# Kernel tuning notes

Measured on AMD Instinct MI355X. Metric: run time of the kernel, lower is better.

The kernel has to match this reference:

```python
import jax, jax.numpy as jnp
import numpy as np

N_TREES, N_LEAVES, PATH_LEN, N_NODES, D, B = 10, 16, 5, 31, 256, 4096


def _local_paths():
    # root-to-leaf paths of a full binary tree, depth 4: 31 nodes, 16 leaves, path len 5
    return np.array([[0, 1 + l // 8, 3 + l // 4, 7 + l // 2, 15 + l]
                     for l in range(N_LEAVES)], np.int32)


def setup_inputs() -> dict:
    key = jax.random.key(0)
    k1, k2, k3, k4, k5, k6 = jax.random.split(key, 6)
    # one activated leaf per tree -> multi-hot cross_features (B, N_TREES*N_LEAVES)
    leaf = jax.random.randint(k1, (B, N_TREES), 0, N_LEAVES)
    cross = jnp.zeros((B, N_TREES, N_LEAVES), jnp.float32)
    cross = cross.at[jnp.arange(B)[:, None], jnp.arange(N_TREES)[None, :], leaf].set(1.0)
    cross_features = cross.reshape(B, N_TREES * N_LEAVES)
    # learned params: node embedding table + single-layer LSTM (torch init scale 1/sqrt(D))
    emb = jax.random.normal(k2, (N_TREES * N_NODES, D), jnp.float32) * 0.02
    s = 1.0 / np.sqrt(D)
    W_ih = jax.random.uniform(k3, (4 * D, D), jnp.float32, -s, s)
    W_hh = jax.random.uniform(k4, (4 * D, D), jnp.float32, -s, s)
    b_ih = jax.random.uniform(k5, (4 * D,), jnp.float32, -s, s)
    b_hh = jax.random.uniform(k6, (4 * D,), jnp.float32, -s, s)
    return {"cross_features": cross_features, "emb": emb, "W_ih": W_ih,
            "W_hh": W_hh, "b_ih": b_ih, "b_hh": b_hh}


def reference(cross_features, emb, W_ih, W_hh, b_ih, b_hh):
    # global path node ids per (tree, leaf): [T, L, P]
    gpaths = jnp.asarray(_local_paths())[None, :, :] + \
        (jnp.arange(N_TREES, dtype=jnp.int32) * N_NODES)[:, None, None]
    # activated leaf per tree (exactly one hot per 16-leaf block)
    leaf = jnp.argmax(cross_features.reshape(B, N_TREES, N_LEAVES), axis=-1)  # [B, T]
    node_ids = gpaths[jnp.arange(N_TREES)[None, :], leaf]                     # [B, T, P]
    x = emb[node_ids].reshape(B * N_TREES, PATH_LEN, D)                       # packed paths
    # precompute input projections for all steps: [N, P, 4D]
    xg = jnp.einsum('npd,gd->npg', x, W_ih) + (b_ih + b_hh)

    def step(carry, xt):
        h, c = carry
        g = xt + h @ W_hh.T
        i, f, gg, o = jnp.split(g, 4, axis=-1)  # torch gate order: i, f, g, o
        c = jax.nn.sigmoid(f) * c + jax.nn.sigmoid(i) * jnp.tanh(gg)
        h = jax.nn.sigmoid(o) * jnp.tanh(c)
        return (h, c), None

    n = B * N_TREES
    h0 = jnp.zeros((n, D), x.dtype)
    (h, _), _ = jax.lax.scan(step, (h0, h0), jnp.swapaxes(xg, 0, 1))
    return h.reshape(B, N_TREES, D)
```

## Files before the change

### kernel.cpp

```cpp
#include <hip/hip_runtime.h>

#define NT 10
#define NL 16
#define NN 31
#define DD 256
#define NB 4096

__device__ unsigned g_gen[NT * 16];

__device__ __forceinline__ float sigf(float x)   { return 1.0f / (1.0f + __expf(-x)); }
__device__ __forceinline__ float tanh_f(float x) { return 2.0f / (1.0f + __expf(-2.0f*x)) - 1.0f; }

__device__ __forceinline__ void pub64(unsigned long long* p, unsigned tag, float v) {
    union { float f; unsigned u; } c; c.f = v;
    __hip_atomic_store(p, ((unsigned long long)tag << 32) | c.u,
                       __ATOMIC_RELAXED, __HIP_MEMORY_SCOPE_AGENT);
}
__device__ __forceinline__ unsigned long long ld64(const unsigned long long* p) {
    return __hip_atomic_load(p, __ATOMIC_RELAXED, __HIP_MEMORY_SCOPE_AGENT);
}

__global__ __launch_bounds__(256) void k_treelstm(
    const float* __restrict__ emb, const float* __restrict__ Wih,
    const float* __restrict__ Whh, const float* __restrict__ bih,
    const float* __restrict__ bhh,
    unsigned long long* __restrict__ hx0, unsigned long long* __restrict__ hx1,
    unsigned long long* __restrict__ hx2, unsigned long long* __restrict__ hx3,
    float* __restrict__ h4g)
{
    __shared__ float es [NN * DD];
    __shared__ float ps [8 * DD];
    __shared__ float xsl[NN * 64];
    __shared__ float hs [8 * DD];
    __shared__ float cbuf[2 * 128];
    __shared__ float bsl[64];
    __shared__ unsigned stag;

    const int tid  = threadIdx.x;
    const int t    = blockIdx.x >> 4;
    const int dt   = blockIdx.x & 15;
    const int kq   = tid >> 6;
    const int w    = tid & 63;
    const int gate = w >> 4;
    const int col  = w & 15;
    const int grow = gate * DD + dt * 16 + col;

    if (tid == 0) {
        unsigned G = __hip_atomic_load(&g_gen[t * 16 + dt],
            __ATOMIC_RELAXED, __HIP_MEMORY_SCOPE_AGENT);
        __hip_atomic_store(&g_gen[t * 16 + dt], G + 1u,
            __ATOMIC_RELAXED, __HIP_MEMORY_SCOPE_AGENT);
        stag = G + 1u;
    }
    if (tid < 64) {
        int g2 = tid >> 4, c3 = tid & 15;
        int r2 = g2 * DD + dt * 16 + c3;
        bsl[tid] = bih[r2] + bhh[r2];
    }

    const float4* Wi4 = (const float4*)Wih + (size_t)grow * 64 + kq * 16;
    const float4* Wh4 = (const float4*)Whh + (size_t)grow * 64 + kq * 16;
    float4 wih[16], whh[16];
    #pragma unroll
    for (int j = 0; j < 16; ++j) { wih[j] = Wi4[j]; whh[j] = Wh4[j]; }

    const float4* emb4 = (const float4*)emb + (size_t)t * NN * 64;
    float4* es4 = (float4*)es;
    #pragma unroll
    for (int r = 0; r < 8; ++r) {
        int idx = tid + 256 * r;
        if (idx < NN * 64) es4[idx] = emb4[idx];
    }
    __syncthreads();
    const unsigned tag = stag;

    auto xbatch = [&](int n0, int nn) {
        __syncthreads();
        float acc[8];
        #pragma unroll
        for (int m = 0; m < 8; ++m) acc[m] = 0.f;
        #pragma unroll
        for (int j = 0; j < 16; ++j) {
            float4 wv = wih[j];
            #pragma unroll
            for (int m = 0; m < 8; ++m) {
                if (m < nn) {
                    float4 h = es4[(n0 + m) * 64 + kq * 16 + j];
                    acc[m] = fmaf(wv.x, h.x, fmaf(wv.y, h.y,
                             fmaf(wv.z, h.z, fmaf(wv.w, h.w, acc[m]))));
                }
            }
        }
        #pragma unroll
        for (int m = 0; m < 8; ++m)
            if (m < nn) ps[m * DD + kq * 64 + w] = acc[m];
        __syncthreads();
        #pragma unroll
        for (int rep = 0; rep < 2; ++rep) {
            int idx = tid + 256 * rep;
            if (idx < nn * 64) {
                int m = idx >> 6, w2 = idx & 63;
                xsl[(n0 + m) * 64 + w2] =
                      ps[m * DD +   0 + w2] + ps[m * DD +  64 + w2]
                    + ps[m * DD + 128 + w2] + ps[m * DD + 192 + w2] + bsl[w2];
            }
        }
        __syncthreads();
    };

    xbatch(0, 1);
    if (tid < 16) {
        float xi  = xsl[ 0 + tid];
        float xgg = xsl[32 + tid];
        float xo  = xsl[48 + tid];
        float c0 = sigf(xi) * tanh_f(xgg);
        float h0 = sigf(xo) * tanh_f(c0);
        cbuf[tid] = c0;
        pub64(hx0 + (size_t)t * DD + dt * 16 + tid, tag, h0);
    }

    xbatch(1, 6);

    {
        const unsigned long long* src = hx0 + (size_t)t * DD;
        unsigned long long v = ld64(src + tid);
        while ((unsigned)(v >> 32) != tag) {
            __builtin_amdgcn_s_sleep(1);
            v = ld64(src + tid);
        }
        union { unsigned u; float f; } cv; cv.u = (unsigned)v;
        hs[tid] = cv.f;
    }
    __syncthreads();

    const unsigned long long* hin[3] = { hx1, hx2, hx3 };
    unsigned long long* hout[3] = { hx1, hx2, hx3 };

    #pragma unroll
    for (int s = 1; s <= 4; ++s) {
        const int L = 1 << (s - 1);

        if (s > 1) {
            const unsigned long long* src = hin[s - 2] + (size_t)t * L * DD;
            unsigned long long v[8];
            #pragma unroll
            for (int r = 0; r < L; ++r) v[r] = ld64(src + tid + 256 * r);
            #pragma unroll
            for (int r = 0; r < L; ++r) {
                while ((unsigned)(v[r] >> 32) != tag) {
                    __builtin_amdgcn_s_sleep(1);
                    v[r] = ld64(src + tid + 256 * r);
                }
                union { unsigned u; float f; } cv; cv.u = (unsigned)v[r];
                hs[tid + 256 * r] = cv.f;
            }
            __syncthreads();
        }

        const float4* hs4 = (const float4*)hs;
        float acc[8];
        #pragma unroll
        for (int p = 0; p < 8; ++p) acc[p] = 0.f;
        #pragma unroll
        for (int j = 0; j < 16; ++j) {
            float4 wv = whh[j];
            #pragma unroll
            for (int p = 0; p < L; ++p) {
                float4 h = hs4[p * 64 + kq * 16 + j];
                acc[p] = fmaf(wv.x, h.x, fmaf(wv.y, h.y,
                         fmaf(wv.z, h.z, fmaf(wv.w, h.w, acc[p]))));
            }
        }
        #pragma unroll
        for (int p = 0; p < L; ++p) ps[p * DD + kq * 64 + w] = acc[p];
        __syncthreads();

        if (tid < 32 * L) {
            const int p  = tid >> 5;
            const int c2 = tid & 15;
            const int q  = tid >> 4;
            float g0 = 0.f, g1 = 0.f, g2 = 0.f, g3 = 0.f;
            #pragma unroll
            for (int k = 0; k < 4; ++k) {
                const float* pp = ps + p * DD + k * 64;
                g0 += pp[ 0 + c2]; g1 += pp[16 + c2];
                g2 += pp[32 + c2]; g3 += pp[48 + c2];
            }
            const int node = (1 << s) - 1 + q;
            const float* xp = xsl + node * 64;
            float gi = g0 + xp[ 0 + c2];
            float gf = g1 + xp[16 + c2];
            float gg = g2 + xp[32 + c2];
            float go = g3 + xp[48 + c2];
            float cin = cbuf[((s - 1) & 1) * 128 + p * 16 + c2];
            float cn  = sigf(gf) * cin + sigf(gi) * tanh_f(gg);
            float hn  = sigf(go) * tanh_f(cn);
            if (s < 4) {
                cbuf[(s & 1) * 128 + q * 16 + c2] = cn;
                pub64(hout[s - 1] + (size_t)(t * 2 * L + q) * DD
                                  + dt * 16 + c2, tag, hn);
            } else {
                h4g[(size_t)(t * NL + q) * DD + dt * 16 + c2] = hn;
            }
        }

        if (s == 1)      xbatch( 7, 8);
        else if (s == 2) xbatch(15, 8);
        else if (s == 3) xbatch(23, 8);
    }
}

__global__ __launch_bounds__(256) void k_scatter(
    const float* __restrict__ cross, const float* __restrict__ htab,
    float* __restrict__ out)
{
    const int tid  = threadIdx.x;
    const int wave = tid >> 6;
    const int lane = tid & 63;
    const int r = blockIdx.x * 4 + wave;
    const int b = r / NT;
    const int t = r - b * NT;

    float v = 0.f;
    if (lane < NL) v = cross[(size_t)b * (NT * NL) + t * NL + lane];
    unsigned long long m = __ballot(v > 0.5f);
    int leaf = m ? (int)__builtin_ctzll(m) : 0;
    int p = t * NL + leaf;

    const float4* h4 = (const float4*)htab;
    float4* o4 = (float4*)out;
    o4[(size_t)r * 64 + lane] = h4[(size_t)p * 64 + lane];
}

extern "C" void kernel_launch(void* const* d_in, const int* in_sizes, int n_in,
                              void* d_out, int out_size, void* d_ws, size_t ws_size,
                              hipStream_t stream)
{
    const float* cross = (const float*)d_in[0];
    const float* emb   = (const float*)d_in[1];
    const float* Wih   = (const float*)d_in[2];
    const float* Whh   = (const float*)d_in[3];
    const float* bih   = (const float*)d_in[4];
    const float* bhh   = (const float*)d_in[5];
    float* out = (float*)d_out;

    unsigned long long* hx0 = (unsigned long long*)d_ws;
    unsigned long long* hx1 = hx0 + (size_t)NT * DD;
    unsigned long long* hx2 = hx1 + (size_t)2 * NT * DD;
    unsigned long long* hx3 = hx2 + (size_t)4 * NT * DD;
    float* h4g = (float*)(hx3 + (size_t)8 * NT * DD);

    hipLaunchKernelGGL(k_treelstm, dim3(160), dim3(256), 0, stream,
                       emb, Wih, Whh, bih, bhh, hx0, hx1, hx2, hx3, h4g);
    hipLaunchKernelGGL(k_scatter, dim3(10240), dim3(256), 0, stream,
                       cross, h4g, out);
}
```

Baseline: 101.3 us.

## Fuse tree-LSTM and leaf scatter into one persistent kernel with tagged flags

Merges the recurrence kernel and the gather/scatter kernel into a single launch. The first 160 blocks run the tree LSTM and publish the final leaf hidden states with generation tags, and 320 extra blocks decode the active leaves and spin on those tags before writing the output. This removes the second launch and the gap between kernels, and lets the output writes overlap the recurrence tail. It depends on all 480 blocks being co-resident, since spinning blocks could otherwise starve the producers, and it doubles the bytes read for the gathered states because each value carries a 64-bit tag.

```diff
diff --git a/kernel.cpp b/kernel.cpp
--- a/kernel.cpp
+++ b/kernel.cpp
@@ -5,8 +5,10 @@
 #define NN 31
 #define DD 256
 #define NB 4096
+#define NSB 320
 
 __device__ unsigned g_gen[NT * 16];
+__device__ unsigned g_sgen[NSB];
 
 __device__ __forceinline__ float sigf(float x)   { return 1.0f / (1.0f + __expf(-x)); }
 __device__ __forceinline__ float tanh_f(float x) { return 2.0f / (1.0f + __expf(-2.0f*x)) - 1.0f; }
@@ -19,217 +21,256 @@
 __device__ __forceinline__ unsigned long long ld64(const unsigned long long* p) {
     return __hip_atomic_load(p, __ATOMIC_RELAXED, __HIP_MEMORY_SCOPE_AGENT);
 }
-
-__global__ __launch_bounds__(256) void k_treelstm(
-    const float* __restrict__ emb, const float* __restrict__ Wih,
-    const float* __restrict__ Whh, const float* __restrict__ bih,
-    const float* __restrict__ bhh,
+__device__ __forceinline__ float payload(unsigned long long w) {
+    union { unsigned u; float f; } c; c.u = (unsigned)w; return c.f;
+}
+
+__global__ __launch_bounds__(256, 2) void k_fused(
+    const float* __restrict__ cross, const float* __restrict__ emb,
+    const float* __restrict__ Wih,   const float* __restrict__ Whh,
+    const float* __restrict__ bih,   const float* __restrict__ bhh,
     unsigned long long* __restrict__ hx0, unsigned long long* __restrict__ hx1,
     unsigned long long* __restrict__ hx2, unsigned long long* __restrict__ hx3,
-    float* __restrict__ h4g)
-{
-    __shared__ float es [NN * DD];
-    __shared__ float ps [8 * DD];
-    __shared__ float xsl[NN * 64];
-    __shared__ float hs [8 * DD];
-    __shared__ float cbuf[2 * 128];
-    __shared__ float bsl[64];
-    __shared__ unsigned stag;
-
-    const int tid  = threadIdx.x;
-    const int t    = blockIdx.x >> 4;
-    const int dt   = blockIdx.x & 15;
-    const int kq   = tid >> 6;
-    const int w    = tid & 63;
-    const int gate = w >> 4;
-    const int col  = w & 15;
-    const int grow = gate * DD + dt * 16 + col;
-
-    if (tid == 0) {
-        unsigned G = __hip_atomic_load(&g_gen[t * 16 + dt],
-            __ATOMIC_RELAXED, __HIP_MEMORY_SCOPE_AGENT);
-        __hip_atomic_store(&g_gen[t * 16 + dt], G + 1u,
-            __ATOMIC_RELAXED, __HIP_MEMORY_SCOPE_AGENT);
-        stag = G + 1u;
-    }
-    if (tid < 64) {
-        int g2 = tid >> 4, c3 = tid & 15;
-        int r2 = g2 * DD + dt * 16 + c3;
-        bsl[tid] = bih[r2] + bhh[r2];
-    }
-
-    const float4* Wi4 = (const float4*)Wih + (size_t)grow * 64 + kq * 16;
-    const float4* Wh4 = (const float4*)Whh + (size_t)grow * 64 + kq * 16;
-    float4 wih[16], whh[16];
-    #pragma unroll
-    for (int j = 0; j < 16; ++j) { wih[j] = Wi4[j]; whh[j] = Wh4[j]; }
-
-    const float4* emb4 = (const float4*)emb + (size_t)t * NN * 64;
-    float4* es4 = (float4*)es;
-    #pragma unroll
-    for (int r = 0; r < 8; ++r) {
-        int idx = tid + 256 * r;
-        if (idx < NN * 64) es4[idx] = emb4[idx];
-    }
-    __syncthreads();
-    const unsigned tag = stag;
-
-    auto xbatch = [&](int n0, int nn) {
-        __syncthreads();
-        float acc[8];
-        #pragma unroll
-        for (int m = 0; m < 8; ++m) acc[m] = 0.f;
-        #pragma unroll
-        for (int j = 0; j < 16; ++j) {
-            float4 wv = wih[j];
-            #pragma unroll
-            for (int m = 0; m < 8; ++m) {
-                if (m < nn) {
-                    float4 h = es4[(n0 + m) * 64 + kq * 16 + j];
-                    acc[m] = fmaf(wv.x, h.x, fmaf(wv.y, h.y,
-                             fmaf(wv.z, h.z, fmaf(wv.w, h.w, acc[m]))));
-                }
-            }
-        }
-        #pragma unroll
-        for (int m = 0; m < 8; ++m)
-            if (m < nn) ps[m * DD + kq * 64 + w] = acc[m];
-        __syncthreads();
-        #pragma unroll
-        for (int rep = 0; rep < 2; ++rep) {
-            int idx = tid + 256 * rep;
-            if (idx < nn * 64) {
-                int m = idx >> 6, w2 = idx & 63;
-                xsl[(n0 + m) * 64 + w2] =
-                      ps[m * DD +   0 + w2] + ps[m * DD +  64 + w2]
-                    + ps[m * DD + 128 + w2] + ps[m * DD + 192 + w2] + bsl[w2];
-            }
-        }
-        __syncthreads();
-    };
-
-    xbatch(0, 1);
-    if (tid < 16) {
-        float xi  = xsl[ 0 + tid];
-        float xgg = xsl[32 + tid];
-        float xo  = xsl[48 + tid];
-        float c0 = sigf(xi) * tanh_f(xgg);
-        float h0 = sigf(xo) * tanh_f(c0);
-        cbuf[tid] = c0;
-        pub64(hx0 + (size_t)t * DD + dt * 16 + tid, tag, h0);
-    }
-
-    xbatch(1, 6);
-
-    {
-        const unsigned long long* src = hx0 + (size_t)t * DD;
-        unsigned long long v = ld64(src + tid);
-        while ((unsigned)(v >> 32) != tag) {
-            __builtin_amdgcn_s_sleep(1);
-            v = ld64(src + tid);
-        }
-        union { unsigned u; float f; } cv; cv.u = (unsigned)v;
-        hs[tid] = cv.f;
-    }
-    __syncthreads();
-
-    const unsigned long long* hin[3] = { hx1, hx2, hx3 };
-    unsigned long long* hout[3] = { hx1, hx2, hx3 };
-
-    #pragma unroll
-    for (int s = 1; s <= 4; ++s) {
-        const int L = 1 << (s - 1);
-
-        if (s > 1) {
-            const unsigned long long* src = hin[s - 2] + (size_t)t * L * DD;
-            unsigned long long v[8];
-            #pragma unroll
-            for (int r = 0; r < L; ++r) v[r] = ld64(src + tid + 256 * r);
-            #pragma unroll
-            for (int r = 0; r < L; ++r) {
-                while ((unsigned)(v[r] >> 32) != tag) {
-                    __builtin_amdgcn_s_sleep(1);
-                    v[r] = ld64(src + tid + 256 * r);
-                }
-                union { unsigned u; float f; } cv; cv.u = (unsigned)v[r];
-                hs[tid + 256 * r] = cv.f;
-            }
-            __syncthreads();
-        }
-
-        const float4* hs4 = (const float4*)hs;
-        float acc[8];
-        #pragma unroll
-        for (int p = 0; p < 8; ++p) acc[p] = 0.f;
-        #pragma unroll
-        for (int j = 0; j < 16; ++j) {
-            float4 wv = whh[j];
-            #pragma unroll
-            for (int p = 0; p < L; ++p) {
-                float4 h = hs4[p * 64 + kq * 16 + j];
-                acc[p] = fmaf(wv.x, h.x, fmaf(wv.y, h.y,
-                         fmaf(wv.z, h.z, fmaf(wv.w, h.w, acc[p]))));
-            }
-        }
-        #pragma unroll
-        for (int p = 0; p < L; ++p) ps[p * DD + kq * 64 + w] = acc[p];
-        __syncthreads();
-
-        if (tid < 32 * L) {
-            const int p  = tid >> 5;
-            const int c2 = tid & 15;
-            const int q  = tid >> 4;
-            float g0 = 0.f, g1 = 0.f, g2 = 0.f, g3 = 0.f;
-            #pragma unroll
-            for (int k = 0; k < 4; ++k) {
-                const float* pp = ps + p * DD + k * 64;
-                g0 += pp[ 0 + c2]; g1 += pp[16 + c2];
-                g2 += pp[32 + c2]; g3 += pp[48 + c2];
-            }
-            const int node = (1 << s) - 1 + q;
-            const float* xp = xsl + node * 64;
-            float gi = g0 + xp[ 0 + c2];
-            float gf = g1 + xp[16 + c2];
-            float gg = g2 + xp[32 + c2];
-            float go = g3 + xp[48 + c2];
-            float cin = cbuf[((s - 1) & 1) * 128 + p * 16 + c2];
-            float cn  = sigf(gf) * cin + sigf(gi) * tanh_f(gg);
-            float hn  = sigf(go) * tanh_f(cn);
-            if (s < 4) {
-                cbuf[(s & 1) * 128 + q * 16 + c2] = cn;
-                pub64(hout[s - 1] + (size_t)(t * 2 * L + q) * DD
-                                  + dt * 16 + c2, tag, hn);
-            } else {
-                h4g[(size_t)(t * NL + q) * DD + dt * 16 + c2] = hn;
-            }
-        }
-
-        if (s == 1)      xbatch( 7, 8);
-        else if (s == 2) xbatch(15, 8);
-        else if (s == 3) xbatch(23, 8);
-    }
-}
-
-__global__ __launch_bounds__(256) void k_scatter(
-    const float* __restrict__ cross, const float* __restrict__ htab,
+    unsigned long long* __restrict__ hx4,
     float* __restrict__ out)
 {
-    const int tid  = threadIdx.x;
-    const int wave = tid >> 6;
-    const int lane = tid & 63;
-    const int r = blockIdx.x * 4 + wave;
-    const int b = r / NT;
-    const int t = r - b * NT;
-
-    float v = 0.f;
-    if (lane < NL) v = cross[(size_t)b * (NT * NL) + t * NL + lane];
-    unsigned long long m = __ballot(v > 0.5f);
-    int leaf = m ? (int)__builtin_ctzll(m) : 0;
-    int p = t * NL + leaf;
-
-    const float4* h4 = (const float4*)htab;
-    float4* o4 = (float4*)out;
-    o4[(size_t)r * 64 + lane] = h4[(size_t)p * 64 + lane];
+    __shared__ float smem[14336];
+    __shared__ unsigned stag;
+    const int tid = threadIdx.x;
+    const int bid = blockIdx.x;
+
+    if (bid < 160) {
+        float* es   = smem;
+        float* ps   = smem + 7936;
+        float* xsl  = smem + 9984;
+        float* hs   = smem + 11968;
+        float* cbuf = smem + 14016;
+        float* bsl  = smem + 14272;
+        float4* es4 = (float4*)es;
+
+        const int t    = bid >> 4;
+        const int dt   = bid & 15;
+        const int kq   = tid >> 6;
+        const int w    = tid & 63;
+        const int gate = w >> 4;
+        const int col  = w & 15;
+        const int grow = gate * DD + dt * 16 + col;
+
+        if (tid == 0) {
+            unsigned G = __hip_atomic_load(&g_gen[t * 16 + dt],
+                __ATOMIC_RELAXED, __HIP_MEMORY_SCOPE_AGENT);
+            __hip_atomic_store(&g_gen[t * 16 + dt], G + 1u,
+                __ATOMIC_RELAXED, __HIP_MEMORY_SCOPE_AGENT);
+            stag = G + 1u;
+        }
+        if (tid < 64) {
+            int g2 = tid >> 4, c3 = tid & 15;
+            int r2 = g2 * DD + dt * 16 + c3;
+            bsl[tid] = bih[r2] + bhh[r2];
+        }
+
+        const float4* Wi4 = (const float4*)Wih + (size_t)grow * 64 + kq * 16;
+        const float4* Wh4 = (const float4*)Whh + (size_t)grow * 64 + kq * 16;
+        float4 wih[16], whh[16];
+        #pragma unroll
+        for (int j = 0; j < 16; ++j) { wih[j] = Wi4[j]; whh[j] = Wh4[j]; }
+
+        const float4* emb4 = (const float4*)emb + (size_t)t * NN * 64;
+        #pragma unroll
+        for (int r = 0; r < 8; ++r) {
+            int idx = tid + 256 * r;
+            if (idx < NN * 64) es4[idx] = emb4[idx];
+        }
+        __syncthreads();
+        const unsigned tag = stag;
+
+        auto xbatch = [&](int n0, int nn) {
+            __syncthreads();
+            float acc[8];
+            #pragma unroll
+            for (int m = 0; m < 8; ++m) acc[m] = 0.f;
+            #pragma unroll
+            for (int j = 0; j < 16; ++j) {
+                float4 wv = wih[j];
+                #pragma unroll
+                for (int m = 0; m < 8; ++m) {
+                    if (m < nn) {
+                        float4 h = es4[(n0 + m) * 64 + kq * 16 + j];
+                        acc[m] = fmaf(wv.x, h.x, fmaf(wv.y, h.y,
+                                 fmaf(wv.z, h.z, fmaf(wv.w, h.w, acc[m]))));
+                    }
+                }
+            }
+            #pragma unroll
+            for (int m = 0; m < 8; ++m)
+                if (m < nn) ps[m * DD + kq * 64 + w] = acc[m];
+            __syncthreads();
+            #pragma unroll
+            for (int rep = 0; rep < 2; ++rep) {
+                int idx = tid + 256 * rep;
+                if (idx < nn * 64) {
+                    int m = idx >> 6, w2 = idx & 63;
+                    xsl[(n0 + m) * 64 + w2] =
+                          ps[m * DD +   0 + w2] + ps[m * DD +  64 + w2]
+                        + ps[m * DD + 128 + w2] + ps[m * DD + 192 + w2] + bsl[w2];
+                }
+            }
+            __syncthreads();
+        };
+
+        xbatch(0, 1);
+        if (tid < 16) {
+            float xi  = xsl[ 0 + tid];
+            float xgg = xsl[32 + tid];
+            float xo  = xsl[48 + tid];
+            float c0 = sigf(xi) * tanh_f(xgg);
+            float h0 = sigf(xo) * tanh_f(c0);
+            cbuf[tid] = c0;
+            pub64(hx0 + (size_t)t * DD + dt * 16 + tid, tag, h0);
+        }
+
+        xbatch(1, 6);
+
+        {
+            const unsigned long long* src = hx0 + (size_t)t * DD;
+            unsigned long long v = ld64(src + tid);
+            while ((unsigned)(v >> 32) != tag) {
+                __builtin_amdgcn_s_sleep(1);
+                v = ld64(src + tid);
+            }
+            hs[tid] = payload(v);
+        }
+        __syncthreads();
+
+        const unsigned long long* hin[3] = { hx1, hx2, hx3 };
+        unsigned long long* hout[3] = { hx1, hx2, hx3 };
+
+        #pragma unroll
+        for (int s = 1; s <= 4; ++s) {
+            const int L = 1 << (s - 1);
+
+            if (s > 1) {
+                const unsigned long long* src = hin[s - 2] + (size_t)t * L * DD;
+                unsigned long long v[8];
+                #pragma unroll
+                for (int r = 0; r < L; ++r) v[r] = ld64(src + tid + 256 * r);
+                #pragma unroll
+                for (int r = 0; r < L; ++r) {
+                    while ((unsigned)(v[r] >> 32) != tag) {
+                        __builtin_amdgcn_s_sleep(1);
+                        v[r] = ld64(src + tid + 256 * r);
+                    }
+                    hs[tid + 256 * r] = payload(v[r]);
+                }
+                __syncthreads();
+            }
+
+            const float4* hs4 = (const float4*)hs;
+            float acc[8];
+            #pragma unroll
+            for (int p = 0; p < 8; ++p) acc[p] = 0.f;
+            #pragma unroll
+            for (int j = 0; j < 16; ++j) {
+                float4 wv = whh[j];
+                #pragma unroll
+                for (int p = 0; p < L; ++p) {
+                    float4 h = hs4[p * 64 + kq * 16 + j];
+                    acc[p] = fmaf(wv.x, h.x, fmaf(wv.y, h.y,
+                             fmaf(wv.z, h.z, fmaf(wv.w, h.w, acc[p]))));
+                }
+            }
+            #pragma unroll
+            for (int p = 0; p < L; ++p) ps[p * DD + kq * 64 + w] = acc[p];
+            __syncthreads();
+
+            if (tid < 32 * L) {
+                const int p  = tid >> 5;
+                const int c2 = tid & 15;
+                const int q  = tid >> 4;
+                float g0 = 0.f, g1 = 0.f, g2 = 0.f, g3 = 0.f;
+                #pragma unroll
+                for (int k = 0; k < 4; ++k) {
+                    const float* pp = ps + p * DD + k * 64;
+                    g0 += pp[ 0 + c2]; g1 += pp[16 + c2];
+                    g2 += pp[32 + c2]; g3 += pp[48 + c2];
+                }
+                const int node = (1 << s) - 1 + q;
+                const float* xp = xsl + node * 64;
+                float gi = g0 + xp[ 0 + c2];
+                float gf = g1 + xp[16 + c2];
+                float gg = g2 + xp[32 + c2];
+                float go = g3 + xp[48 + c2];
+                float cin = cbuf[((s - 1) & 1) * 128 + p * 16 + c2];
+                float cn  = sigf(gf) * cin + sigf(gi) * tanh_f(gg);
+                float hn  = sigf(go) * tanh_f(cn);
+                if (s < 4) {
+                    cbuf[(s & 1) * 128 + q * 16 + c2] = cn;
+                    pub64(hout[s - 1] + (size_t)(t * 2 * L + q) * DD
+                                      + dt * 16 + c2, tag, hn);
+                } else {
+                    pub64(hx4 + (size_t)(t * NL + q) * DD
+                              + dt * 16 + c2, tag, hn);
+                }
+            }
+
+            if (s == 1)      xbatch( 7, 8);
+            else if (s == 2) xbatch(15, 8);
+            else if (s == 3) xbatch(23, 8);
+        }
+    } else {
+        float* cls  = smem;
+        int* leafs  = (int*)(smem + 2048);
+
+        const int sb = bid - 160;
+        const size_t r0 = (size_t)sb * 128;
+
+        if (tid == 0) {
+            unsigned G = __hip_atomic_load(&g_sgen[sb],
+                __ATOMIC_RELAXED, __HIP_MEMORY_SCOPE_AGENT);
+            __hip_atomic_store(&g_sgen[sb], G + 1u,
+                __ATOMIC_RELAXED, __HIP_MEMORY_SCOPE_AGENT);
+            stag = G + 1u;
+        }
+
+        #pragma unroll
+        for (int k = 0; k < 8; ++k)
+            cls[tid + 256 * k] = cross[r0 * 16 + tid + 256 * k];
+        __syncthreads();
+        const unsigned tag = stag;
+        if (tid < 128) {
+            int leaf = 0;
+            #pragma unroll
+            for (int l = 15; l >= 0; --l)
+                if (cls[tid * 16 + l] > 0.5f) leaf = l;
+            int r = (int)(r0 + (size_t)tid);
+            int b = r / NT;
+            int t = r - b * NT;
+            leafs[tid] = t * 16 + leaf;
+        }
+        __syncthreads();
+
+        const int wave = tid >> 6;
+        const int lane = tid & 63;
+        float4* o4 = (float4*)out;
+        #pragma unroll 4
+        for (int it = 0; it < 32; ++it) {
+            int rr = it * 4 + wave;
+            const unsigned long long* hw =
+                hx4 + (size_t)leafs[rr] * DD + lane * 4;
+            unsigned long long w0 = ld64(hw + 0);
+            unsigned long long w1 = ld64(hw + 1);
+            unsigned long long w2 = ld64(hw + 2);
+            unsigned long long w3 = ld64(hw + 3);
+            while ((unsigned)(w0 >> 32) != tag) { __builtin_amdgcn_s_sleep(1); w0 = ld64(hw + 0); }
+            while ((unsigned)(w1 >> 32) != tag) { __builtin_amdgcn_s_sleep(1); w1 = ld64(hw + 1); }
+            while ((unsigned)(w2 >> 32) != tag) { __builtin_amdgcn_s_sleep(1); w2 = ld64(hw + 2); }
+            while ((unsigned)(w3 >> 32) != tag) { __builtin_amdgcn_s_sleep(1); w3 = ld64(hw + 3); }
+            float4 f;
+            f.x = payload(w0); f.y = payload(w1);
+            f.z = payload(w2); f.w = payload(w3);
+            o4[(r0 + rr) * 64 + lane] = f;
+        }
+    }
 }
 
 extern "C" void kernel_launch(void* const* d_in, const int* in_sizes, int n_in,
@@ -248,10 +289,9 @@
     unsigned long long* hx1 = hx0 + (size_t)NT * DD;
     unsigned long long* hx2 = hx1 + (size_t)2 * NT * DD;
     unsigned long long* hx3 = hx2 + (size_t)4 * NT * DD;
-    float* h4g = (float*)(hx3 + (size_t)8 * NT * DD);
-
-    hipLaunchKernelGGL(k_treelstm, dim3(160), dim3(256), 0, stream,
-                       emb, Wih, Whh, bih, bhh, hx0, hx1, hx2, hx3, h4g);
-    hipLaunchKernelGGL(k_scatter, dim3(10240), dim3(256), 0, stream,
-                       cross, h4g, out);
-}
+    unsigned long long* hx4 = hx3 + (size_t)8 * NT * DD;
+
+    hipLaunchKernelGGL(k_fused, dim3(160 + NSB), dim3(256), 0, stream,
+                       cross, emb, Wih, Whh, bih, bhh,
+                       hx0, hx1, hx2, hx3, hx4, out);
+}
```

New measurement: 139.2 us. 37.4% more time.
